# Performance work log

Measured on AMD Instinct MI355X. Metric: run time of the kernel, lower is better.

The kernel has to match this reference:

```python
import jax, jax.numpy as jnp
import numpy as np

D_MODEL = 2048
N_HEADS = 16
D_K = D_MODEL // N_HEADS  # 128


def setup_inputs() -> dict:
    key = jax.random.key(0)
    ks = jax.random.split(key, 12)
    B, S = 2, 2048
    std = 1.0 / np.sqrt(D_MODEL)
    inp = {
        "query": jax.random.normal(ks[0], (B, S, D_MODEL), jnp.float32),
        "key": jax.random.normal(ks[1], (B, S, D_MODEL), jnp.float32),
        "value": jax.random.normal(ks[2], (B, S, D_MODEL), jnp.float32),
        "w_q": jax.random.normal(ks[3], (D_MODEL, D_MODEL), jnp.float32) * std,
        "b_q": jnp.zeros((D_MODEL,), jnp.float32),
        "w_k": jax.random.normal(ks[4], (D_MODEL, D_MODEL), jnp.float32) * std,
        "b_k": jnp.zeros((D_MODEL,), jnp.float32),
        "w_v": jax.random.normal(ks[5], (D_MODEL, D_MODEL), jnp.float32) * std,
        "b_v": jnp.zeros((D_MODEL,), jnp.float32),
        "w_o": jax.random.normal(ks[6], (D_MODEL, D_MODEL), jnp.float32) * std,
        "b_o": jnp.zeros((D_MODEL,), jnp.float32),
        # fractional scale numerator / denominator per head; ratio ~ 1/sqrt(d_k)
        "scale_alpha": jnp.full((N_HEADS,), 1.0, jnp.float32),
        "scale_beta": jnp.full((N_HEADS,), float(np.sqrt(D_K)), jnp.float32),
    }
    return inp


def reference(query, key, value, w_q, b_q, w_k, b_k, w_v, b_v, w_o, b_o,
              scale_alpha, scale_beta):
    B, S, _ = query.shape
    # projections (torch Linear: x @ W^T + b)
    Q = (query @ w_q.T + b_q).reshape(B, S, N_HEADS, D_K).transpose(0, 2, 1, 3)
    K = (key @ w_k.T + b_k).reshape(B, S, N_HEADS, D_K).transpose(0, 2, 1, 3)
    V = (value @ w_v.T + b_v).reshape(B, S, N_HEADS, D_K).transpose(0, 2, 1, 3)
    # per-head fractional scale alpha/beta (computed under no_grad in torch)
    scales = jax.lax.stop_gradient(scale_alpha / jnp.maximum(scale_beta, 1.0))
    scores = jnp.einsum("bhqd,bhkd->bhqk", Q, K) * scales[None, :, None, None]
    attn = jax.nn.softmax(scores, axis=-1)  # dropout is identity in eval
    out = jnp.einsum("bhqk,bhkd->bhqd", attn, V)
    out = out.transpose(0, 2, 1, 3).reshape(B, S, D_MODEL)
    return out @ w_o.T + b_o
```

## Files before the change

### kernel.cpp

```cpp
#include <hip/hip_runtime.h>
#include <cstdint>

#define S_LEN   2048
#define DMODEL  2048
#define NHEADS  16
#define DK      128
#define MROWS   4096

typedef _Float16 f16;
using f16x8 = __attribute__((ext_vector_type(8))) _Float16;
using f16x4 = __attribute__((ext_vector_type(4))) _Float16;
using f32x4 = __attribute__((ext_vector_type(4))) float;

typedef const __attribute__((address_space(1))) unsigned int gu32;
typedef __attribute__((address_space(3))) unsigned int lu32;

__device__ __forceinline__ void gl2lds16(const void* g, void* l) {
    __builtin_amdgcn_global_load_lds((gu32*)g, (lu32*)l, 16, 0, 0);
}

__global__ __launch_bounds__(256) void cvt_all(
    const float* __restrict__ q, const float* __restrict__ k,
    const float* __restrict__ v, const float* __restrict__ wq,
    const float* __restrict__ wk, const float* __restrict__ wv,
    const float* __restrict__ wo,
    f16* cq, f16* ck, f16* cv, f16* cwq, f16* cwk, f16* cwv, f16* cwo)
{
    const int b = blockIdx.x;
    const float* src; f16* dst; int base;
    if      (b <  8192) { src = q;  dst = cq;  base = b; }
    else if (b < 16384) { src = k;  dst = ck;  base = b - 8192; }
    else if (b < 24576) { src = v;  dst = cv;  base = b - 16384; }
    else if (b < 28672) { src = wq; dst = cwq; base = b - 24576; }
    else if (b < 32768) { src = wk; dst = cwk; base = b - 28672; }
    else if (b < 36864) { src = wv; dst = cwv; base = b - 32768; }
    else                { src = wo; dst = cwo; base = b - 36864; }
    const int i = base * 256 + threadIdx.x;
    float4 x = ((const float4*)src)[i];
    f16x4 o; o[0] = (f16)x.x; o[1] = (f16)x.y; o[2] = (f16)x.z; o[3] = (f16)x.w;
    ((f16x4*)dst)[i] = o;
}

__device__ __forceinline__ void gemm_core(
    const f16* __restrict__ A, const f16* __restrict__ W,
    const float* __restrict__ bias, void* __restrict__ Cout,
    int mode, const float* __restrict__ sa, const float* __restrict__ sb)
{
    __shared__ f16 As[128 * 32];
    __shared__ f16 Bs[128 * 32];

    const int tid = threadIdx.x;
    const int bm = blockIdx.y * 128;
    const int bn = blockIdx.x * 128;
    const int wid = tid >> 6;
    const int ln = tid & 15;
    const int quad = (tid & 63) >> 4;
    const int wm = (wid >> 1) * 64;
    const int wn = (wid & 1) * 64;
    const int K = DMODEL, N = DMODEL;

    f32x4 acc[4][4];
#pragma unroll
    for (int i = 0; i < 4; ++i)
#pragma unroll
        for (int j = 0; j < 4; ++j)
            acc[i][j] = (f32x4){0.f, 0.f, 0.f, 0.f};

    const int sr = tid >> 2;
    const int ke = (tid & 3) * 8;
    const f16* ga0 = A + (size_t)(bm + sr) * K + ke;
    const f16* ga1 = A + (size_t)(bm + 64 + sr) * K + ke;
    const f16* gb0 = W + (size_t)(bn + sr) * K + ke;
    const f16* gb1 = W + (size_t)(bn + 64 + sr) * K + ke;
    f16* la0 = As + tid * 8;
    f16* la1 = As + 2048 + tid * 8;
    f16* lb0 = Bs + tid * 8;
    f16* lb1 = Bs + 2048 + tid * 8;

    for (int k0 = 0; k0 < K; k0 += 32) {
        __syncthreads();
        gl2lds16(ga0 + k0, la0);
        gl2lds16(ga1 + k0, la1);
        gl2lds16(gb0 + k0, lb0);
        gl2lds16(gb1 + k0, lb1);
        __syncthreads();

        f16x8 af[4], bf[4];
#pragma unroll
        for (int i = 0; i < 4; ++i)
            af[i] = *(const f16x8*)&As[(wm + i * 16 + ln) * 32 + quad * 8];
#pragma unroll
        for (int j = 0; j < 4; ++j)
            bf[j] = *(const f16x8*)&Bs[(wn + j * 16 + ln) * 32 + quad * 8];
#pragma unroll
        for (int i = 0; i < 4; ++i)
#pragma unroll
            for (int j = 0; j < 4; ++j)
                acc[i][j] = __builtin_amdgcn_mfma_f32_16x16x32_f16(
                    af[i], bf[j], acc[i][j], 0, 0, 0);
    }

#pragma unroll
    for (int j = 0; j < 4; ++j) {
        const int n = bn + wn + j * 16 + ln;
        const float bn_ = bias[n];
        const int h = n >> 7;
        const int d = n & (DK - 1);
        float scq = 1.0f;
        if (mode == 3) scq = sa[h] / fmaxf(sb[h], 1.0f);
#pragma unroll
        for (int i = 0; i < 4; ++i) {
#pragma unroll
            for (int reg = 0; reg < 4; ++reg) {
                const int m = bm + wm + i * 16 + quad * 4 + reg;
                float v = acc[i][j][reg] + bn_;
                if (mode == 0) {
                    ((float*)Cout)[(size_t)m * N + n] = v;
                } else {
                    const int bb = m >> 11;
                    const int ss = m & (S_LEN - 1);
                    size_t idx;
                    if (mode == 2)
                        idx = (((size_t)(bb * NHEADS + h) * DK + d) * S_LEN + ss);
                    else
                        idx = (((size_t)(bb * NHEADS + h) * S_LEN + ss) * DK + d);
                    if (mode == 3) v *= scq;
                    ((f16*)Cout)[idx] = (f16)v;
                }
            }
        }
    }
}

__global__ __launch_bounds__(256) void qkv_gemm(
    const f16* Aq, const f16* Ak, const f16* Av,
    const f16* Wq, const f16* Wk, const f16* Wv,
    const float* bq, const float* bk, const float* bv,
    f16* Oq, f16* Ok, f16* Ov, const float* sa, const float* sb)
{
    const int z = blockIdx.z;
    const f16* A = (z == 0) ? Aq : (z == 1) ? Ak : Av;
    const f16* W = (z == 0) ? Wq : (z == 1) ? Wk : Wv;
    const float* bias = (z == 0) ? bq : (z == 1) ? bk : bv;
    void* O = (z == 0) ? (void*)Oq : (z == 1) ? (void*)Ok : (void*)Ov;
    const int mode = (z == 0) ? 3 : (z == 1) ? 1 : 2;
    gemm_core(A, W, bias, O, mode, sa, sb);
}

__global__ __launch_bounds__(256) void out_gemm(
    const f16* A, const f16* W, const float* bias, float* O)
{
    gemm_core(A, W, bias, O, 0, nullptr, nullptr);
}

__global__ __launch_bounds__(256, 2) void flash_v4(
    const f16* __restrict__ Qg, const f16* __restrict__ Kg,
    const f16* __restrict__ VTg, f16* __restrict__ AO)
{
    __shared__ f16 Ks[4 * 64 * 32];
    __shared__ f16 Vs[2 * 128 * 32];
    __shared__ f16 Ps[2 * 128 * 32];
    __shared__ float l_buf[2 * 128];

    const int tid = threadIdx.x;
    const int wid = tid >> 6;
    const int ln = tid & 15;
    const int quad = (tid & 63) >> 4;
    const int wq = wid & 1;
    const int wc = wid >> 1;
    const int bh = blockIdx.y;
    const int q0 = blockIdx.x * 128;

    f16x8 qf[4][4];
    const f16* Qbase = Qg + ((size_t)bh * S_LEN + q0 + wq * 64) * DK;
#pragma unroll
    for (int nt = 0; nt < 4; ++nt)
#pragma unroll
        for (int kc = 0; kc < 4; ++kc)
            qf[nt][kc] = *(const f16x8*)(Qbase + (size_t)(nt * 16 + ln) * DK
                                         + kc * 32 + quad * 8);

    f32x4 o[4][4];
    float lp[4] = {0.f, 0.f, 0.f, 0.f};
#pragma unroll
    for (int i = 0; i < 4; ++i)
#pragma unroll
        for (int j = 0; j < 4; ++j)
            o[i][j] = (f32x4){0.f, 0.f, 0.f, 0.f};

    const f16* Kgb = Kg + (size_t)bh * S_LEN * DK;
    const f16* Vgb = VTg + (size_t)bh * DK * S_LEN;
    const int srow = tid >> 2;
    const int soff = (tid & 3) * 8;

    for (int kt = 0; kt < S_LEN / 64; ++kt) {
        __syncthreads();
#pragma unroll
        for (int j = 0; j < 4; ++j)
            gl2lds16(Kgb + (size_t)(kt * 64 + srow) * DK + j * 32 + soff,
                     Ks + j * 2048 + tid * 8);
#pragma unroll
        for (int j = 0; j < 4; ++j)
            gl2lds16(Vgb + (size_t)(srow + (j & 1) * 64) * S_LEN
                         + kt * 64 + (j >> 1) * 32 + soff,
                     Vs + (j >> 1) * 4096 + (j & 1) * 2048 + tid * 8);
        __syncthreads();

        f32x4 s[2][4];
#pragma unroll
        for (int mt = 0; mt < 2; ++mt)
#pragma unroll
            for (int nt = 0; nt < 4; ++nt)
                s[mt][nt] = (f32x4){0.f, 0.f, 0.f, 0.f};
#pragma unroll
        for (int kc = 0; kc < 4; ++kc) {
            f16x8 kf0 = *(const f16x8*)&Ks[kc * 2048 + (wc * 32 + ln) * 32 + quad * 8];
            f16x8 kf1 = *(const f16x8*)&Ks[kc * 2048 + (wc * 32 + 16 + ln) * 32 + quad * 8];
#pragma unroll
            for (int nt = 0; nt < 4; ++nt) {
                s[0][nt] = __builtin_amdgcn_mfma_f32_16x16x32_f16(kf0, qf[nt][kc], s[0][nt], 0, 0, 0);
                s[1][nt] = __builtin_amdgcn_mfma_f32_16x16x32_f16(kf1, qf[nt][kc], s[1][nt], 0, 0, 0);
            }
        }

#pragma unroll
        for (int mt = 0; mt < 2; ++mt) {
#pragma unroll
            for (int nt = 0; nt < 4; ++nt) {
                const float p0 = __expf(s[mt][nt][0]);
                const float p1 = __expf(s[mt][nt][1]);
                const float p2 = __expf(s[mt][nt][2]);
                const float p3 = __expf(s[mt][nt][3]);
                lp[nt] += (p0 + p1) + (p2 + p3);
                f16x4 pk;
                pk[0] = (f16)p0; pk[1] = (f16)p1; pk[2] = (f16)p2; pk[3] = (f16)p3;
                *(f16x4*)&Ps[wc * 4096 + (wq * 64 + nt * 16 + ln) * 32
                             + mt * 16 + quad * 4] = pk;
            }
        }
        __syncthreads();

#pragma unroll
        for (int cc = 0; cc < 2; ++cc) {
            f16x8 pf[4];
#pragma unroll
            for (int mtq = 0; mtq < 4; ++mtq)
                pf[mtq] = *(const f16x8*)&Ps[cc * 4096 + (wq * 64 + mtq * 16 + ln) * 32 + quad * 8];
#pragma unroll
            for (int ntd = 0; ntd < 4; ++ntd) {
                f16x8 vf = *(const f16x8*)&Vs[cc * 4096 + (wc * 64 + ntd * 16 + ln) * 32 + quad * 8];
#pragma unroll
                for (int mtq = 0; mtq < 4; ++mtq)
                    o[mtq][ntd] = __builtin_amdgcn_mfma_f32_16x16x32_f16(
                        pf[mtq], vf, o[mtq][ntd], 0, 0, 0);
            }
        }
    }

#pragma unroll
    for (int nt = 0; nt < 4; ++nt) {
        float v = lp[nt];
        v += __shfl_xor(v, 16, 64);
        v += __shfl_xor(v, 32, 64);
        lp[nt] = v;
    }
    if (quad == 0) {
#pragma unroll
        for (int nt = 0; nt < 4; ++nt)
            l_buf[wc * 128 + wq * 64 + nt * 16 + ln] = lp[nt];
    }
    __syncthreads();

    const int b = bh >> 4;
    const int h = bh & (NHEADS - 1);
#pragma unroll
    for (int mtq = 0; mtq < 4; ++mtq) {
#pragma unroll
        for (int reg = 0; reg < 4; ++reg) {
            const int ql = wq * 64 + mtq * 16 + quad * 4 + reg;
            const float inv = 1.0f / (l_buf[ql] + l_buf[128 + ql]);
            f16* dst = AO + ((size_t)b * S_LEN + q0 + ql) * DMODEL + h * DK + wc * 64;
#pragma unroll
            for (int ntd = 0; ntd < 4; ++ntd)
                dst[ntd * 16 + ln] = (f16)(o[mtq][ntd][reg] * inv);
        }
    }
}

extern "C" void kernel_launch(void* const* d_in, const int* in_sizes, int n_in,
                              void* d_out, int out_size, void* d_ws, size_t ws_size,
                              hipStream_t stream)
{
    (void)in_sizes; (void)n_in; (void)out_size; (void)ws_size;
    const float* query = (const float*)d_in[0];
    const float* key_  = (const float*)d_in[1];
    const float* value = (const float*)d_in[2];
    const float* w_q = (const float*)d_in[3];
    const float* b_q = (const float*)d_in[4];
    const float* w_k = (const float*)d_in[5];
    const float* b_k = (const float*)d_in[6];
    const float* w_v = (const float*)d_in[7];
    const float* b_v = (const float*)d_in[8];
    const float* w_o = (const float*)d_in[9];
    const float* b_o = (const float*)d_in[10];
    const float* s_alpha = (const float*)d_in[11];
    const float* s_beta  = (const float*)d_in[12];
    float* out = (float*)d_out;

    const size_t T = (size_t)MROWS * DMODEL;
    const size_t Wn = (size_t)DMODEL * DMODEL;
    f16* base = (f16*)d_ws;
    f16* c_q = base;
    f16* c_k = base + T;
    f16* c_v = base + 2 * T;
    f16* Qh  = base + 3 * T;
    f16* wq16 = base + 4 * T;
    f16* wk16 = wq16 + Wn;
    f16* wv16 = wk16 + Wn;
    f16* wo16 = wv16 + Wn;
    f16* Kh  = c_q;
    f16* VT  = c_k;
    f16* AOh = c_v;

    dim3 blk(256);

    cvt_all<<<dim3(40960), blk, 0, stream>>>(query, key_, value, w_q, w_k, w_v, w_o,
                                             c_q, c_k, c_v, wq16, wk16, wv16, wo16);

    dim3 qkv_grid(DMODEL / 128, MROWS / 128, 3);
    qkv_gemm<<<qkv_grid, blk, 0, stream>>>(c_q, c_k, c_v, wq16, wk16, wv16,
                                           b_q, b_k, b_v, Qh, Kh, VT,
                                           s_alpha, s_beta);

    dim3 flash_grid(S_LEN / 128, 2 * NHEADS);
    flash_v4<<<flash_grid, blk, 0, stream>>>(Qh, Kh, VT, AOh);

    dim3 out_grid(DMODEL / 128, MROWS / 128);
    out_gemm<<<out_grid, blk, 0, stream>>>(AOh, wo16, b_o, out);
}
```

Measured before the change: 500.1 us.

## Switch projection GEMMs to 32x32 MFMA with swizzled block order and vector V store

The projection GEMM core moves from 16x16x32 MFMA tiles to 32x32x16 MFMA tiles, which cuts the number of LDS fragment loads per MFMA. Blocks are remapped from a 2D grid to a 1D index that groups pairs of N-tiles across all M-tiles, aiming for better L2 reuse of A and W. The transposed V output is now written as packed f16x4 stores along the sequence dimension. The fused three-way QKV launch is split into three separate launches of 512 blocks each, which adds launch overhead and loses concurrency across the three projections.

```diff
diff --git a/kernel.cpp b/kernel.cpp
--- a/kernel.cpp
+++ b/kernel.cpp
@@ -11,6 +11,7 @@
 using f16x8 = __attribute__((ext_vector_type(8))) _Float16;
 using f16x4 = __attribute__((ext_vector_type(4))) _Float16;
 using f32x4 = __attribute__((ext_vector_type(4))) float;
+using f32x16 = __attribute__((ext_vector_type(16))) float;
 
 typedef const __attribute__((address_space(1))) unsigned int gu32;
 typedef __attribute__((address_space(3))) unsigned int lu32;
@@ -44,27 +45,29 @@
 __device__ __forceinline__ void gemm_core(
     const f16* __restrict__ A, const f16* __restrict__ W,
     const float* __restrict__ bias, void* __restrict__ Cout,
-    int mode, const float* __restrict__ sa, const float* __restrict__ sb)
+    int bmb, int bnb, int mode,
+    const float* __restrict__ sa, const float* __restrict__ sb)
 {
     __shared__ f16 As[128 * 32];
     __shared__ f16 Bs[128 * 32];
 
     const int tid = threadIdx.x;
-    const int bm = blockIdx.y * 128;
-    const int bn = blockIdx.x * 128;
+    const int bm = bmb * 128;
+    const int bn = bnb * 128;
     const int wid = tid >> 6;
-    const int ln = tid & 15;
-    const int quad = (tid & 63) >> 4;
+    const int ln31 = tid & 31;
+    const int ln5 = (tid & 63) >> 5;
     const int wm = (wid >> 1) * 64;
     const int wn = (wid & 1) * 64;
     const int K = DMODEL, N = DMODEL;
 
-    f32x4 acc[4][4];
-#pragma unroll
-    for (int i = 0; i < 4; ++i)
-#pragma unroll
-        for (int j = 0; j < 4; ++j)
-            acc[i][j] = (f32x4){0.f, 0.f, 0.f, 0.f};
+    f32x16 acc[2][2];
+#pragma unroll
+    for (int i = 0; i < 2; ++i)
+#pragma unroll
+        for (int j = 0; j < 2; ++j)
+#pragma unroll
+            for (int r = 0; r < 16; ++r) acc[i][j][r] = 0.0f;
 
     const int sr = tid >> 2;
     const int ke = (tid & 3) * 8;
@@ -85,72 +88,77 @@
         gl2lds16(gb1 + k0, lb1);
         __syncthreads();
 
-        f16x8 af[4], bf[4];
-#pragma unroll
-        for (int i = 0; i < 4; ++i)
-            af[i] = *(const f16x8*)&As[(wm + i * 16 + ln) * 32 + quad * 8];
-#pragma unroll
-        for (int j = 0; j < 4; ++j)
-            bf[j] = *(const f16x8*)&Bs[(wn + j * 16 + ln) * 32 + quad * 8];
-#pragma unroll
-        for (int i = 0; i < 4; ++i)
-#pragma unroll
-            for (int j = 0; j < 4; ++j)
-                acc[i][j] = __builtin_amdgcn_mfma_f32_16x16x32_f16(
-                    af[i], bf[j], acc[i][j], 0, 0, 0);
-    }
-
-#pragma unroll
-    for (int j = 0; j < 4; ++j) {
-        const int n = bn + wn + j * 16 + ln;
+#pragma unroll
+        for (int s = 0; s < 2; ++s) {
+            f16x8 af[2], bf[2];
+#pragma unroll
+            for (int i = 0; i < 2; ++i)
+                af[i] = *(const f16x8*)&As[(wm + i * 32 + ln31) * 32 + s * 16 + ln5 * 8];
+#pragma unroll
+            for (int j = 0; j < 2; ++j)
+                bf[j] = *(const f16x8*)&Bs[(wn + j * 32 + ln31) * 32 + s * 16 + ln5 * 8];
+#pragma unroll
+            for (int i = 0; i < 2; ++i)
+#pragma unroll
+                for (int j = 0; j < 2; ++j)
+                    acc[i][j] = __builtin_amdgcn_mfma_f32_32x32x16_f16(
+                        af[i], bf[j], acc[i][j], 0, 0, 0);
+        }
+    }
+
+#pragma unroll
+    for (int j = 0; j < 2; ++j) {
+        const int n = bn + wn + j * 32 + ln31;
         const float bn_ = bias[n];
         const int h = n >> 7;
         const int d = n & (DK - 1);
         float scq = 1.0f;
         if (mode == 3) scq = sa[h] / fmaxf(sb[h], 1.0f);
 #pragma unroll
-        for (int i = 0; i < 4; ++i) {
-#pragma unroll
-            for (int reg = 0; reg < 4; ++reg) {
-                const int m = bm + wm + i * 16 + quad * 4 + reg;
-                float v = acc[i][j][reg] + bn_;
-                if (mode == 0) {
-                    ((float*)Cout)[(size_t)m * N + n] = v;
+        for (int i = 0; i < 2; ++i) {
+#pragma unroll
+            for (int rg = 0; rg < 4; ++rg) {
+                const int m0 = bm + wm + i * 32 + rg * 8 + ln5 * 4;
+                if (mode == 2) {
+                    const int bb = m0 >> 11;
+                    const int ss = m0 & (S_LEN - 1);
+                    f16x4 pk;
+#pragma unroll
+                    for (int r = 0; r < 4; ++r)
+                        pk[r] = (f16)(acc[i][j][rg * 4 + r] + bn_);
+                    *(f16x4*)&((f16*)Cout)[(((size_t)(bb * NHEADS + h) * DK + d)
+                                            * S_LEN + ss)] = pk;
                 } else {
-                    const int bb = m >> 11;
-                    const int ss = m & (S_LEN - 1);
-                    size_t idx;
-                    if (mode == 2)
-                        idx = (((size_t)(bb * NHEADS + h) * DK + d) * S_LEN + ss);
-                    else
-                        idx = (((size_t)(bb * NHEADS + h) * S_LEN + ss) * DK + d);
-                    if (mode == 3) v *= scq;
-                    ((f16*)Cout)[idx] = (f16)v;
+#pragma unroll
+                    for (int r = 0; r < 4; ++r) {
+                        const int m = m0 + r;
+                        float v = acc[i][j][rg * 4 + r] + bn_;
+                        if (mode == 0) {
+                            ((float*)Cout)[(size_t)m * N + n] = v;
+                        } else {
+                            const int bb = m >> 11;
+                            const int ss = m & (S_LEN - 1);
+                            if (mode == 3) v *= scq;
+                            ((f16*)Cout)[(((size_t)(bb * NHEADS + h) * S_LEN + ss)
+                                          * DK + d)] = (f16)v;
+                        }
+                    }
                 }
             }
         }
     }
 }
 
-__global__ __launch_bounds__(256) void qkv_gemm(
-    const f16* Aq, const f16* Ak, const f16* Av,
-    const f16* Wq, const f16* Wk, const f16* Wv,
-    const float* bq, const float* bk, const float* bv,
-    f16* Oq, f16* Ok, f16* Ov, const float* sa, const float* sb)
-{
-    const int z = blockIdx.z;
-    const f16* A = (z == 0) ? Aq : (z == 1) ? Ak : Av;
-    const f16* W = (z == 0) ? Wq : (z == 1) ? Wk : Wv;
-    const float* bias = (z == 0) ? bq : (z == 1) ? bk : bv;
-    void* O = (z == 0) ? (void*)Oq : (z == 1) ? (void*)Ok : (void*)Ov;
-    const int mode = (z == 0) ? 3 : (z == 1) ? 1 : 2;
-    gemm_core(A, W, bias, O, mode, sa, sb);
-}
-
-__global__ __launch_bounds__(256) void out_gemm(
-    const f16* A, const f16* W, const float* bias, float* O)
-{
-    gemm_core(A, W, bias, O, 0, nullptr, nullptr);
+__global__ __launch_bounds__(256) void proj_gemm(
+    const f16* A, const f16* W, const float* bias, void* O,
+    int mode, const float* sa, const float* sb)
+{
+    const int id = blockIdx.x;
+    const int x = id & 7;
+    const int t = id >> 3;
+    const int bn = x * 2 + (t >> 5);
+    const int bm = t & 31;
+    gemm_core(A, W, bias, O, bm, bn, mode, sa, sb);
 }
 
 __global__ __launch_bounds__(256, 2) void flash_v4(
@@ -327,14 +335,12 @@
     cvt_all<<<dim3(40960), blk, 0, stream>>>(query, key_, value, w_q, w_k, w_v, w_o,
                                              c_q, c_k, c_v, wq16, wk16, wv16, wo16);
 
-    dim3 qkv_grid(DMODEL / 128, MROWS / 128, 3);
-    qkv_gemm<<<qkv_grid, blk, 0, stream>>>(c_q, c_k, c_v, wq16, wk16, wv16,
-                                           b_q, b_k, b_v, Qh, Kh, VT,
-                                           s_alpha, s_beta);
+    proj_gemm<<<dim3(512), blk, 0, stream>>>(c_q, wq16, b_q, Qh, 3, s_alpha, s_beta);
+    proj_gemm<<<dim3(512), blk, 0, stream>>>(c_k, wk16, b_k, Kh, 1, nullptr, nullptr);
+    proj_gemm<<<dim3(512), blk, 0, stream>>>(c_v, wv16, b_v, VT, 2, nullptr, nullptr);
 
     dim3 flash_grid(S_LEN / 128, 2 * NHEADS);
     flash_v4<<<flash_grid, blk, 0, stream>>>(Qh, Kh, VT, AOh);
 
-    dim3 out_grid(DMODEL / 128, MROWS / 128);
-    out_gemm<<<out_grid, blk, 0, stream>>>(AOh, wo16, b_o, out);
-}
+    proj_gemm<<<dim3(512), blk, 0, stream>>>(AOh, wo16, b_o, out, 0, nullptr, nullptr);
+}
```

After: 523.6 us. +4.7%, slower.
